# Optimization experiments

Hardware: AMD Instinct MI355X
Metric: run time of the kernel (lower is better)

Reference implementation:

```python
import jax, jax.numpy as jnp
import numpy as np

N, E, F_IN, H, L = 50000, 600000, 256, 128, 3
EPS = 1e-5


def setup_inputs() -> dict:
    key = jax.random.key(0)
    ks = jax.random.split(key, 10)
    x = jax.random.normal(ks[0], (N, F_IN), dtype=jnp.float32)
    edge_index = jax.random.randint(ks[1], (2, E), 0, N, dtype=jnp.int64)
    # BatchNorm params init per module: weight=1, bias=1e-4
    bn_feat_g = jnp.ones((F_IN,), jnp.float32)
    bn_feat_b = jnp.full((F_IN,), 1e-4, jnp.float32)
    bns_g = jnp.ones((L, H), jnp.float32)
    bns_b = jnp.full((L, H), 1e-4, jnp.float32)
    # conv_feat (gfn=True: pure linear) weight/bias, glorot-ish scale
    Wf = jax.random.normal(ks[2], (F_IN, H), dtype=jnp.float32) * (1.0 / np.sqrt(F_IN))
    bf = jnp.zeros((H,), jnp.float32)
    Ws = jax.random.normal(ks[3], (L, H, H), dtype=jnp.float32) * (1.0 / np.sqrt(H))
    bs = jnp.zeros((L, H), jnp.float32)
    return {"x": x, "edge_index": edge_index, "bn_feat_g": bn_feat_g,
            "bn_feat_b": bn_feat_b, "Wf": Wf, "bf": bf,
            "bns_g": bns_g, "bns_b": bns_b, "Ws": Ws, "bs": bs}


def _batchnorm(x, g, b):
    # training-mode BN over the node dimension
    mu = jnp.mean(x, axis=0)
    var = jnp.mean((x - mu) ** 2, axis=0)
    return (x - mu) * jax.lax.rsqrt(var + EPS) * g + b


def reference(x, edge_index, bn_feat_g, bn_feat_b, Wf, bf, bns_g, bns_b, Ws, bs):
    n = x.shape[0]
    src, dst = edge_index[0], edge_index[1]
    # add self loops once; compute symmetric GCN normalization
    loops = jnp.arange(n, dtype=edge_index.dtype)
    src_f = jnp.concatenate([src, loops])
    dst_f = jnp.concatenate([dst, loops])
    deg = jax.ops.segment_sum(jnp.ones_like(dst_f, dtype=x.dtype), dst_f, num_segments=n)
    dinv = jax.lax.rsqrt(jnp.maximum(deg, 1.0))
    norm = dinv[src_f] * dinv[dst_f]  # [E+N]

    def gcn_conv(h, W, b_):
        h = h @ W
        msg = norm[:, None] * h[src_f]          # gather + scale per edge
        out = jax.ops.segment_sum(msg, dst_f, num_segments=n)  # scatter-add
        return out + b_

    h = _batchnorm(x, bn_feat_g, bn_feat_b)
    h = jax.nn.relu(h @ Wf + bf)                # conv_feat with gfn=True: no propagation
    for i in range(L):
        h = _batchnorm(h, bns_g[i], bns_b[i])
        h = gcn_conv(h, Ws[i], bs[i])
        if i == L - 1:
            break
        h = jax.nn.relu(h)
    # inner-product link scoring on the original (no self-loop) edges
    link_score = jax.nn.sigmoid(jnp.sum(h[src] * h[dst], axis=1))
    return link_score
```

## Files before the change

### kernel.cpp

```cpp
#include <hip/hip_runtime.h>
#include <cstdint>
#include <cstddef>

#define F_INC 256
#define HDIM 128
#define NLAYER 3
#define EPSV 1e-5f

__global__ void detect_i64_kernel(const long long* __restrict__ p, int E, int N,
                                  int* __restrict__ flag) {
  int i = blockIdx.x * blockDim.x + threadIdx.x;
  if (i < E) {
    long long v = p[i];
    if (v < 0 || v >= (long long)N) atomicOr(flag, 1);
  }
}

__global__ void convert_idx_kernel(const void* __restrict__ p, int E,
                                   const int* __restrict__ flag,
                                   int* __restrict__ src32, int* __restrict__ dst32) {
  int i = blockIdx.x * blockDim.x + threadIdx.x;
  if (i >= E) return;
  if (*flag == 0) {
    const long long* q = (const long long*)p;
    src32[i] = (int)q[i];
    dst32[i] = (int)q[E + i];
  } else {
    const int* q = (const int*)p;
    src32[i] = q[i];
    dst32[i] = q[E + i];
  }
}

template<int F>
__global__ void bn_stats_kernel(const float* __restrict__ h, int nrows, int rowsPerBlock,
                                float* __restrict__ sums ) {
  int f  = threadIdx.x % F;
  int rl = threadIdx.x / F;
  const int R = 256 / F;
  int r0 = blockIdx.x * rowsPerBlock;
  int r1 = min(r0 + rowsPerBlock, nrows);
  float s = 0.f, q = 0.f;
  for (int r = r0 + rl; r < r1; r += R) {
    float v = h[(size_t)r * F + f];
    s += v; q += v * v;
  }
  atomicAdd(&sums[f], s);
  atomicAdd(&sums[F + f], q);
}

template<int F>
__global__ void bn_finalize_kernel(const float* __restrict__ sums, const float* __restrict__ g,
                                   const float* __restrict__ b, int nrows,
                                   float* __restrict__ svec, float* __restrict__ shvec) {
  int f = threadIdx.x;
  float mean = sums[f] / (float)nrows;
  float var  = sums[F + f] / (float)nrows - mean * mean;
  var = fmaxf(var, 0.f);
  float sc = g[f] * rsqrtf(var + EPSV);
  svec[f]  = sc;
  shvec[f] = b[f] - mean * sc;
}

__global__ void fold_bias_kernel(const float* __restrict__ shvec, const float* __restrict__ W,
                                 int K, const float* __restrict__ base, float* __restrict__ cvec) {
  int j = threadIdx.x;
  float acc = base ? base[j] : 0.f;
  for (int k = 0; k < K; ++k) acc += shvec[k] * W[(size_t)k * HDIM + j];
  cvec[j] = acc;
}

template<int K, bool RELU>
__launch_bounds__(256)
__global__ void gemm_affine_kernel(const float* __restrict__ A, const float* __restrict__ W,
                                   const float* __restrict__ svec,
                                   const float* __restrict__ bias, float* __restrict__ out, int nrows) {
  __shared__ float As[16][64];
  __shared__ float Bs[16][128];
  const int t  = threadIdx.x;
  const int tc = t & 31;
  const int tr = t >> 5;
  const int rowBase = blockIdx.x * 64;

  float acc[8][4];
#pragma unroll
  for (int i = 0; i < 8; ++i)
#pragma unroll
    for (int j = 0; j < 4; ++j) acc[i][j] = 0.f;

  const int lrow = t >> 2;
  const int lk   = (t & 3) * 4;

  for (int k0 = 0; k0 < K; k0 += 16) {
    {
      int gr = rowBase + lrow;
      float4 v;
      if (gr < nrows) {
        v = *(const float4*)&A[(size_t)gr * K + (k0 + lk)];
        float4 sv = *(const float4*)&svec[k0 + lk];
        v.x *= sv.x; v.y *= sv.y; v.z *= sv.z; v.w *= sv.w;
      } else {
        v = make_float4(0.f, 0.f, 0.f, 0.f);
      }
      As[lk + 0][lrow] = v.x;
      As[lk + 1][lrow] = v.y;
      As[lk + 2][lrow] = v.z;
      As[lk + 3][lrow] = v.w;
    }
#pragma unroll
    for (int i = 0; i < 2; ++i) {
      int idx  = t + i * 256;
      int krow = idx >> 5;
      int c    = (idx & 31) * 4;
      *(float4*)&Bs[krow][c] = *(const float4*)&W[(size_t)(k0 + krow) * HDIM + c];
    }
    __syncthreads();
#pragma unroll
    for (int kk = 0; kk < 16; ++kk) {
      float4 a0 = *(const float4*)&As[kk][tr * 8];
      float4 a1 = *(const float4*)&As[kk][tr * 8 + 4];
      float4 b  = *(const float4*)&Bs[kk][tc * 4];
      float ar[8] = {a0.x, a0.y, a0.z, a0.w, a1.x, a1.y, a1.z, a1.w};
      float bc[4] = {b.x, b.y, b.z, b.w};
#pragma unroll
      for (int i = 0; i < 8; ++i)
#pragma unroll
        for (int j = 0; j < 4; ++j) acc[i][j] += ar[i] * bc[j];
    }
    __syncthreads();
  }

  float4 bv = *(const float4*)&bias[tc * 4];
#pragma unroll
  for (int i = 0; i < 8; ++i) {
    int gr = rowBase + tr * 8 + i;
    if (gr < nrows) {
      float4 o;
      o.x = acc[i][0] + bv.x;
      o.y = acc[i][1] + bv.y;
      o.z = acc[i][2] + bv.z;
      o.w = acc[i][3] + bv.w;
      if (RELU) {
        o.x = fmaxf(o.x, 0.f); o.y = fmaxf(o.y, 0.f);
        o.z = fmaxf(o.z, 0.f); o.w = fmaxf(o.w, 0.f);
      }
      *(float4*)&out[(size_t)gr * HDIM + tc * 4] = o;
    }
  }
}

__global__ void init_deg_kernel(float* __restrict__ deg, int n) {
  int i = blockIdx.x * blockDim.x + threadIdx.x;
  if (i < n) deg[i] = 1.0f;
}
__global__ void deg_atomic_kernel(const int* __restrict__ dst, float* __restrict__ deg, int E) {
  int e = blockIdx.x * blockDim.x + threadIdx.x;
  if (e < E) atomicAdd(&deg[dst[e]], 1.0f);
}
__global__ void dinv_kernel(float* __restrict__ deg, int n) {
  int i = blockIdx.x * blockDim.x + threadIdx.x;
  if (i < n) deg[i] = rsqrtf(fmaxf(deg[i], 1.0f));
}

__global__ __launch_bounds__(1024)
void scan_offsets_kernel(const float* __restrict__ deg, int n,
                         int* __restrict__ offs, int* __restrict__ cursor) {
  __shared__ int woff_s[16];
  __shared__ int btot;
  __shared__ int carry;
  const int t = threadIdx.x;
  const int lane = t & 63;
  const int wv = t >> 6;
  if (t == 0) carry = 0;
  __syncthreads();
  for (int base = 0; base < n; base += 1024) {
    int i = base + t;
    int v = (i < n) ? ((int)(deg[i] + 0.5f) - 1) : 0;
    int incl = v;
#pragma unroll
    for (int o = 1; o < 64; o <<= 1) {
      int y = __shfl_up(incl, o);
      if (lane >= o) incl += y;
    }
    if (lane == 63) woff_s[wv] = incl;
    __syncthreads();
    if (t < 16) {
      int x = woff_s[t];
      int xin = x;
#pragma unroll
      for (int o = 1; o < 16; o <<= 1) {
        int y = __shfl_up(xin, o);
        if (t >= o) xin += y;
      }
      woff_s[t] = xin - x;
      if (t == 15) btot = xin;
    }
    __syncthreads();
    int excl = carry + woff_s[wv] + (incl - v);
    if (i < n) { offs[i] = excl; cursor[i] = excl; }
    __syncthreads();
    if (t == 0) carry += btot;
    __syncthreads();
  }
  if (t == 0) offs[n] = carry;
}

__global__ void csr_fill_kernel(const int* __restrict__ src, const int* __restrict__ dst,
                                const float* __restrict__ dinv, int* __restrict__ cursor,
                                int* __restrict__ eperm, float* __restrict__ wperm, int E) {
  int e = blockIdx.x * blockDim.x + threadIdx.x;
  if (e >= E) return;
  int s = src[e], d = dst[e];
  int slot = atomicAdd(&cursor[d], 1);
  eperm[slot] = s;
  wperm[slot] = dinv[s] * dinv[d];
}

__global__ __launch_bounds__(256)
void gcn_gather_kernel(const float* __restrict__ t, const int* __restrict__ offs,
                       const int* __restrict__ eperm, const float* __restrict__ wperm,
                       const float* __restrict__ dinv, const float* __restrict__ bias,
                       float* __restrict__ out, int n, int relu) {
  int gw = (int)((blockIdx.x * blockDim.x + threadIdx.x) >> 6);
  int lane = threadIdx.x & 63;
  if (gw >= n) return;
  float w0 = dinv[gw]; w0 *= w0;
  float2 tv = *(const float2*)&t[(size_t)gw * HDIM + lane * 2];
  float ax = w0 * tv.x, ay = w0 * tv.y;
  int e = offs[gw], e1 = offs[gw + 1];
  for (; e + 1 < e1; e += 2) {
    int s0 = eperm[e], s1 = eperm[e + 1];
    float wa = wperm[e], wb = wperm[e + 1];
    float2 v0 = *(const float2*)&t[(size_t)s0 * HDIM + lane * 2];
    float2 v1 = *(const float2*)&t[(size_t)s1 * HDIM + lane * 2];
    ax += wa * v0.x + wb * v1.x;
    ay += wa * v0.y + wb * v1.y;
  }
  if (e < e1) {
    int s0 = eperm[e]; float wa = wperm[e];
    float2 v0 = *(const float2*)&t[(size_t)s0 * HDIM + lane * 2];
    ax += wa * v0.x; ay += wa * v0.y;
  }
  float2 bv = *(const float2*)&bias[lane * 2];
  ax += bv.x; ay += bv.y;
  if (relu) { ax = fmaxf(ax, 0.f); ay = fmaxf(ay, 0.f); }
  float2 o; o.x = ax; o.y = ay;
  *(float2*)&out[(size_t)gw * HDIM + lane * 2] = o;
}

__global__ void edge_score_kernel(const int* __restrict__ src, const int* __restrict__ dst,
                                  const float* __restrict__ h, float* __restrict__ out, int E) {
  int g = blockIdx.x * blockDim.x + threadIdx.x;
  int e = g >> 6;
  int l = g & 63;
  if (e >= E) return;
  int s = src[e], d = dst[e];
  const float* hs = &h[(size_t)s * HDIM];
  const float* hd = &h[(size_t)d * HDIM];
  float sum = hs[l] * hd[l] + hs[l + 64] * hd[l + 64];
#pragma unroll
  for (int off = 32; off >= 1; off >>= 1) sum += __shfl_xor(sum, off);
  if (l == 0) out[e] = 1.0f / (1.0f + expf(-sum));
}

extern "C" void kernel_launch(void* const* d_in, const int* in_sizes, int n_in,
                              void* d_out, int out_size, void* d_ws, size_t ws_size,
                              hipStream_t stream) {
  const float* x     = (const float*)d_in[0];
  const void*  ei    = d_in[1];
  const float* bn_g  = (const float*)d_in[2];
  const float* bn_b  = (const float*)d_in[3];
  const float* Wf    = (const float*)d_in[4];
  const float* bf    = (const float*)d_in[5];
  const float* bns_g = (const float*)d_in[6];
  const float* bns_b = (const float*)d_in[7];
  const float* Ws    = (const float*)d_in[8];
  const float* bs    = (const float*)d_in[9];
  float* score_out   = (float*)d_out;

  const int N = in_sizes[0] / F_INC;
  const int E = in_sizes[1] / 2;

  const size_t nh = (size_t)N * HDIM;
  float* ws     = (float*)d_ws;
  float* bufA   = ws;
  float* bufB   = bufA + nh;
  float* bufC   = bufB + nh;
  float* dinv   = bufC + nh;
  float* sums   = dinv + N;
  float* svec   = sums + 2 * F_INC;
  float* shvec  = svec + F_INC;
  float* cvec   = shvec + F_INC;
  int*   src    = (int*)(cvec + HDIM);
  int*   dst    = src + E;
  int*   flag   = dst + E;
  int*   offs   = flag + 1;
  int*   cursor = offs + (N + 1);
  int*   eperm  = cursor + N;
  float* wperm  = (float*)(eperm + E);

  const int nB = (N + 255) / 256;
  const int eB = (E + 255) / 256;
  const int gB = (N + 63) / 64;
  const int rpb = (N + 255) / 256;
  const int gatherB = (N + 3) / 4;

  hipMemsetAsync(flag, 0, sizeof(int), stream);
  detect_i64_kernel<<<eB, 256, 0, stream>>>((const long long*)ei, E, N, flag);
  convert_idx_kernel<<<eB, 256, 0, stream>>>(ei, E, flag, src, dst);

  init_deg_kernel<<<nB, 256, 0, stream>>>(dinv, N);
  deg_atomic_kernel<<<eB, 256, 0, stream>>>(dst, dinv, E);
  scan_offsets_kernel<<<1, 1024, 0, stream>>>(dinv, N, offs, cursor);
  dinv_kernel<<<nB, 256, 0, stream>>>(dinv, N);
  csr_fill_kernel<<<eB, 256, 0, stream>>>(src, dst, dinv, cursor, eperm, wperm, E);

  hipMemsetAsync(sums, 0, 2 * F_INC * sizeof(float), stream);
  bn_stats_kernel<F_INC><<<256, 256, 0, stream>>>(x, N, rpb, sums);
  bn_finalize_kernel<F_INC><<<1, F_INC, 0, stream>>>(sums, bn_g, bn_b, N, svec, shvec);
  fold_bias_kernel<<<1, HDIM, 0, stream>>>(shvec, Wf, F_INC, bf, cvec);
  gemm_affine_kernel<F_INC, true><<<gB, 256, 0, stream>>>(x, Wf, svec, cvec, bufA, N);

  float* h    = bufA;
  float* tbuf = bufB;
  float* obuf = bufC;

  for (int i = 0; i < NLAYER; ++i) {
    const float* Wi = Ws + (size_t)i * HDIM * HDIM;
    hipMemsetAsync(sums, 0, 2 * HDIM * sizeof(float), stream);
    bn_stats_kernel<HDIM><<<256, 256, 0, stream>>>(h, N, rpb, sums);
    bn_finalize_kernel<HDIM><<<1, HDIM, 0, stream>>>(sums, bns_g + i * HDIM, bns_b + i * HDIM,
                                                     N, svec, shvec);
    fold_bias_kernel<<<1, HDIM, 0, stream>>>(shvec, Wi, HDIM, nullptr, cvec);
    gemm_affine_kernel<HDIM, false><<<gB, 256, 0, stream>>>(h, Wi, svec, cvec, tbuf, N);
    gcn_gather_kernel<<<gatherB, 256, 0, stream>>>(tbuf, offs, eperm, wperm, dinv,
                                                   bs + i * HDIM, obuf, N,
                                                   (i < NLAYER - 1) ? 1 : 0);
    float* tmp = h;
    h = obuf;
    obuf = tmp;
  }

  {
    long long tt = (long long)E * 64;
    int eb2 = (int)((tt + 255) / 256);
    edge_score_kernel<<<eb2, 256, 0, stream>>>(src, dst, h, score_out, E);
  }
}
```

Before: 1.134 ms.

## Enlarge GEMM tile, fuse BN finalize with bias fold, unroll gather by four

The GEMM now computes a 128x128 output tile per block with an 8x8 per-thread micro-tile and a K step of 8, instead of 64x128 with 8x4. This raises arithmetic intensity per shared-memory load but doubles accumulator registers and halves the block count. BN finalize and bias folding are merged into one kernel that keeps the shift vector in shared memory, removing one launch per layer. The gather loop is unrolled to four edges so more independent loads are in flight.

```diff
diff --git a/kernel.cpp b/kernel.cpp
--- a/kernel.cpp
+++ b/kernel.cpp
@@ -49,102 +49,103 @@
   atomicAdd(&sums[F + f], q);
 }
 
-template<int F>
-__global__ void bn_finalize_kernel(const float* __restrict__ sums, const float* __restrict__ g,
+template<int K>
+__global__ void bn_fin_fold_kernel(const float* __restrict__ sums, const float* __restrict__ g,
                                    const float* __restrict__ b, int nrows,
-                                   float* __restrict__ svec, float* __restrict__ shvec) {
-  int f = threadIdx.x;
-  float mean = sums[f] / (float)nrows;
-  float var  = sums[F + f] / (float)nrows - mean * mean;
+                                   const float* __restrict__ W, const float* __restrict__ base,
+                                   float* __restrict__ svec, float* __restrict__ cvec) {
+  __shared__ float sh[K];
+  int t = threadIdx.x;
+  float mean = sums[t] / (float)nrows;
+  float var  = sums[K + t] / (float)nrows - mean * mean;
   var = fmaxf(var, 0.f);
-  float sc = g[f] * rsqrtf(var + EPSV);
-  svec[f]  = sc;
-  shvec[f] = b[f] - mean * sc;
-}
-
-__global__ void fold_bias_kernel(const float* __restrict__ shvec, const float* __restrict__ W,
-                                 int K, const float* __restrict__ base, float* __restrict__ cvec) {
-  int j = threadIdx.x;
-  float acc = base ? base[j] : 0.f;
-  for (int k = 0; k < K; ++k) acc += shvec[k] * W[(size_t)k * HDIM + j];
-  cvec[j] = acc;
+  float sc = g[t] * rsqrtf(var + EPSV);
+  svec[t] = sc;
+  sh[t] = b[t] - mean * sc;
+  __syncthreads();
+  if (t < HDIM) {
+    float acc = base ? base[t] : 0.f;
+#pragma unroll 8
+    for (int k = 0; k < K; ++k) acc += sh[k] * W[(size_t)k * HDIM + t];
+    cvec[t] = acc;
+  }
 }
 
 template<int K, bool RELU>
 __launch_bounds__(256)
 __global__ void gemm_affine_kernel(const float* __restrict__ A, const float* __restrict__ W,
                                    const float* __restrict__ svec,
-                                   const float* __restrict__ bias, float* __restrict__ out, int nrows) {
-  __shared__ float As[16][64];
-  __shared__ float Bs[16][128];
+                                   const float* __restrict__ bias, float* __restrict__ out,
+                                   int nrows) {
+  __shared__ float As[8][128];
+  __shared__ float Bs[8][128];
   const int t  = threadIdx.x;
-  const int tc = t & 31;
-  const int tr = t >> 5;
-  const int rowBase = blockIdx.x * 64;
-
-  float acc[8][4];
+  const int tx = t & 15;
+  const int ty = t >> 4;
+  const int rowBase = blockIdx.x * 128;
+
+  float acc[8][8];
 #pragma unroll
   for (int i = 0; i < 8; ++i)
 #pragma unroll
-    for (int j = 0; j < 4; ++j) acc[i][j] = 0.f;
-
-  const int lrow = t >> 2;
-  const int lk   = (t & 3) * 4;
-
-  for (int k0 = 0; k0 < K; k0 += 16) {
+    for (int j = 0; j < 8; ++j) acc[i][j] = 0.f;
+
+  const int arow = t >> 1;
+  const int akk  = (t & 1) * 4;
+  const int bkk  = t >> 5;
+  const int bc   = (t & 31) * 4;
+
+  for (int k0 = 0; k0 < K; k0 += 8) {
     {
-      int gr = rowBase + lrow;
-      float4 v;
+      int gr = rowBase + arow;
+      float4 v = make_float4(0.f, 0.f, 0.f, 0.f);
       if (gr < nrows) {
-        v = *(const float4*)&A[(size_t)gr * K + (k0 + lk)];
-        float4 sv = *(const float4*)&svec[k0 + lk];
+        v = *(const float4*)&A[(size_t)gr * K + (k0 + akk)];
+        float4 sv = *(const float4*)&svec[k0 + akk];
         v.x *= sv.x; v.y *= sv.y; v.z *= sv.z; v.w *= sv.w;
-      } else {
-        v = make_float4(0.f, 0.f, 0.f, 0.f);
       }
-      As[lk + 0][lrow] = v.x;
-      As[lk + 1][lrow] = v.y;
-      As[lk + 2][lrow] = v.z;
-      As[lk + 3][lrow] = v.w;
-    }
-#pragma unroll
-    for (int i = 0; i < 2; ++i) {
-      int idx  = t + i * 256;
-      int krow = idx >> 5;
-      int c    = (idx & 31) * 4;
-      *(float4*)&Bs[krow][c] = *(const float4*)&W[(size_t)(k0 + krow) * HDIM + c];
-    }
-    __syncthreads();
-#pragma unroll
-    for (int kk = 0; kk < 16; ++kk) {
-      float4 a0 = *(const float4*)&As[kk][tr * 8];
-      float4 a1 = *(const float4*)&As[kk][tr * 8 + 4];
-      float4 b  = *(const float4*)&Bs[kk][tc * 4];
+      As[akk + 0][arow] = v.x;
+      As[akk + 1][arow] = v.y;
+      As[akk + 2][arow] = v.z;
+      As[akk + 3][arow] = v.w;
+    }
+    *(float4*)&Bs[bkk][bc] = *(const float4*)&W[(size_t)(k0 + bkk) * HDIM + bc];
+    __syncthreads();
+#pragma unroll
+    for (int kk = 0; kk < 8; ++kk) {
+      float4 a0 = *(const float4*)&As[kk][ty * 8];
+      float4 a1 = *(const float4*)&As[kk][ty * 8 + 4];
+      float4 b0 = *(const float4*)&Bs[kk][tx * 8];
+      float4 b1 = *(const float4*)&Bs[kk][tx * 8 + 4];
       float ar[8] = {a0.x, a0.y, a0.z, a0.w, a1.x, a1.y, a1.z, a1.w};
-      float bc[4] = {b.x, b.y, b.z, b.w};
+      float br[8] = {b0.x, b0.y, b0.z, b0.w, b1.x, b1.y, b1.z, b1.w};
 #pragma unroll
       for (int i = 0; i < 8; ++i)
 #pragma unroll
-        for (int j = 0; j < 4; ++j) acc[i][j] += ar[i] * bc[j];
-    }
-    __syncthreads();
-  }
-
-  float4 bv = *(const float4*)&bias[tc * 4];
+        for (int j = 0; j < 8; ++j) acc[i][j] += ar[i] * br[j];
+    }
+    __syncthreads();
+  }
+
+  float4 bv0 = *(const float4*)&bias[tx * 8];
+  float4 bv1 = *(const float4*)&bias[tx * 8 + 4];
 #pragma unroll
   for (int i = 0; i < 8; ++i) {
-    int gr = rowBase + tr * 8 + i;
+    int gr = rowBase + ty * 8 + i;
     if (gr < nrows) {
-      float4 o;
-      o.x = acc[i][0] + bv.x;
-      o.y = acc[i][1] + bv.y;
-      o.z = acc[i][2] + bv.z;
-      o.w = acc[i][3] + bv.w;
+      float4 o0, o1;
+      o0.x = acc[i][0] + bv0.x; o0.y = acc[i][1] + bv0.y;
+      o0.z = acc[i][2] + bv0.z; o0.w = acc[i][3] + bv0.w;
+      o1.x = acc[i][4] + bv1.x; o1.y = acc[i][5] + bv1.y;
+      o1.z = acc[i][6] + bv1.z; o1.w = acc[i][7] + bv1.w;
       if (RELU) {
-        o.x = fmaxf(o.x, 0.f); o.y = fmaxf(o.y, 0.f);
-        o.z = fmaxf(o.z, 0.f); o.w = fmaxf(o.w, 0.f);
+        o0.x = fmaxf(o0.x, 0.f); o0.y = fmaxf(o0.y, 0.f);
+        o0.z = fmaxf(o0.z, 0.f); o0.w = fmaxf(o0.w, 0.f);
+        o1.x = fmaxf(o1.x, 0.f); o1.y = fmaxf(o1.y, 0.f);
+        o1.z = fmaxf(o1.z, 0.f); o1.w = fmaxf(o1.w, 0.f);
       }
-      *(float4*)&out[(size_t)gr * HDIM + tc * 4] = o;
+      *(float4*)&out[(size_t)gr * HDIM + tx * 8]     = o0;
+      *(float4*)&out[(size_t)gr * HDIM + tx * 8 + 4] = o1;
     }
   }
 }
@@ -228,15 +229,17 @@
   float2 tv = *(const float2*)&t[(size_t)gw * HDIM + lane * 2];
   float ax = w0 * tv.x, ay = w0 * tv.y;
   int e = offs[gw], e1 = offs[gw + 1];
-  for (; e + 1 < e1; e += 2) {
-    int s0 = eperm[e], s1 = eperm[e + 1];
-    float wa = wperm[e], wb = wperm[e + 1];
+  for (; e + 3 < e1; e += 4) {
+    int s0 = eperm[e], s1 = eperm[e + 1], s2 = eperm[e + 2], s3 = eperm[e + 3];
+    float wa = wperm[e], wb = wperm[e + 1], wc = wperm[e + 2], wd = wperm[e + 3];
     float2 v0 = *(const float2*)&t[(size_t)s0 * HDIM + lane * 2];
     float2 v1 = *(const float2*)&t[(size_t)s1 * HDIM + lane * 2];
-    ax += wa * v0.x + wb * v1.x;
-    ay += wa * v0.y + wb * v1.y;
-  }
-  if (e < e1) {
+    float2 v2 = *(const float2*)&t[(size_t)s2 * HDIM + lane * 2];
+    float2 v3 = *(const float2*)&t[(size_t)s3 * HDIM + lane * 2];
+    ax += wa * v0.x + wb * v1.x + wc * v2.x + wd * v3.x;
+    ay += wa * v0.y + wb * v1.y + wc * v2.y + wd * v3.y;
+  }
+  for (; e < e1; ++e) {
     int s0 = eperm[e]; float wa = wperm[e];
     float2 v0 = *(const float2*)&t[(size_t)s0 * HDIM + lane * 2];
     ax += wa * v0.x; ay += wa * v0.y;
@@ -301,7 +304,7 @@
 
   const int nB = (N + 255) / 256;
   const int eB = (E + 255) / 256;
-  const int gB = (N + 63) / 64;
+  const int gB = (N + 127) / 128;
   const int rpb = (N + 255) / 256;
   const int gatherB = (N + 3) / 4;
 
@@ -317,8 +320,7 @@
 
   hipMemsetAsync(sums, 0, 2 * F_INC * sizeof(float), stream);
   bn_stats_kernel<F_INC><<<256, 256, 0, stream>>>(x, N, rpb, sums);
-  bn_finalize_kernel<F_INC><<<1, F_INC, 0, stream>>>(sums, bn_g, bn_b, N, svec, shvec);
-  fold_bias_kernel<<<1, HDIM, 0, stream>>>(shvec, Wf, F_INC, bf, cvec);
+  bn_fin_fold_kernel<F_INC><<<1, F_INC, 0, stream>>>(sums, bn_g, bn_b, N, Wf, bf, svec, cvec);
   gemm_affine_kernel<F_INC, true><<<gB, 256, 0, stream>>>(x, Wf, svec, cvec, bufA, N);
 
   float* h    = bufA;
@@ -329,9 +331,8 @@
     const float* Wi = Ws + (size_t)i * HDIM * HDIM;
     hipMemsetAsync(sums, 0, 2 * HDIM * sizeof(float), stream);
     bn_stats_kernel<HDIM><<<256, 256, 0, stream>>>(h, N, rpb, sums);
-    bn_finalize_kernel<HDIM><<<1, HDIM, 0, stream>>>(sums, bns_g + i * HDIM, bns_b + i * HDIM,
-                                                     N, svec, shvec);
-    fold_bias_kernel<<<1, HDIM, 0, stream>>>(shvec, Wi, HDIM, nullptr, cvec);
+    bn_fin_fold_kernel<HDIM><<<1, HDIM, 0, stream>>>(sums, bns_g + i * HDIM, bns_b + i * HDIM,
+                                                     N, Wi, nullptr, svec, cvec);
     gemm_affine_kernel<HDIM, false><<<gB, 256, 0, stream>>>(h, Wi, svec, cvec, tbuf, N);
     gcn_gather_kernel<<<gatherB, 256, 0, stream>>>(tbuf, offs, eperm, wperm, dinv,
                                                    bs + i * HDIM, obuf, N,
```

Result: faster. 959.5 us (-15.4%).
